# Kernel optimization log

Measured on AMD Instinct MI355X. Metric: run time of the kernel, lower is better.

The kernel has to match this reference:

```python
import jax, jax.numpy as jnp
import numpy as np

N = 8192
NFEAT = 784
NUM_CLASSES = 10


def _glorot(key, shape):
    lim = 1.0 / np.sqrt(shape[0])
    return jax.random.uniform(key, shape, jnp.float32, -lim, lim)


def setup_inputs() -> dict:
    key = jax.random.key(0)
    ks = jax.random.split(key, 16)
    x = jax.random.normal(ks[0], (N, NFEAT), jnp.float32)
    adj = (jax.random.uniform(ks[1], (N, N)) < 0.02).astype(jnp.float32)
    adj = jnp.maximum(adj, jnp.eye(N, dtype=jnp.float32))
    dims = [(NFEAT, 256), (256, 128), (256, 256), (128, 128), (128, 128),
            (128, 64), (128, 128), (128, 128), (128, 1)]
    names = ['gcn1', 'd11', 'd12', 'gcn2', 'd21', 'd22', 'gcn3', 'd31', 'd32']
    inp = {'x': x, 'adj': adj}
    for i, (nm, (fi, fo)) in enumerate(zip(names, dims)):
        inp['W_' + nm] = _glorot(ks[2 + i], (fi, fo))
        inp['b_' + nm] = jnp.zeros((fo,), jnp.float32)
    inp['W_fc'] = _glorot(ks[11], (128, NUM_CLASSES))
    inp['b_fc'] = jnp.zeros((NUM_CLASSES,), jnp.float32)
    return inp


def _gcn(x, adj, W, b):
    # Kipf GCN layer: adj @ (x @ W) + b
    return adj @ (x @ W) + b


def _normalize_adj(adj):
    # degree[i,i] = 1/nnz(row_i); out = sqrt(D) @ adj @ sqrt(D)
    deg = jnp.sum(adj != 0, axis=1).astype(adj.dtype)  # [N]
    d = jax.lax.rsqrt(deg)                              # 1/sqrt(deg)
    return adj * d[:, None] * d[None, :]


def reference(x, adj,
              W_gcn1, b_gcn1, W_d11, b_d11, W_d12, b_d12,
              W_gcn2, b_gcn2, W_d21, b_d21, W_d22, b_d22,
              W_gcn3, b_gcn3, W_d31, b_d31, W_d32, b_d32,
              W_fc, b_fc):
    adj = _normalize_adj(adj)
    x = _gcn(x, adj, W_gcn1, b_gcn1)                  # [N, 256]
    z1 = _gcn(x, adj, W_d11, b_d11)                   # [N, 128]
    s1 = jax.nn.softmax(_gcn(x, adj, W_d12, b_d12), axis=1)  # [N, 256]
    x = s1.T @ z1                                     # [256, 128]
    adj = s1.T @ adj @ s1                             # [256, 256]
    x = _gcn(x, adj, W_gcn2, b_gcn2)                  # [256, 128]
    z2 = _gcn(x, adj, W_d21, b_d21)                   # [256, 128]
    s2 = jax.nn.softmax(_gcn(x, adj, W_d22, b_d22), axis=1)  # [256, 64]
    x = s2.T @ z2                                     # [64, 128]
    adj = s2.T @ (adj @ s2)                           # [64, 64]
    x = _gcn(x, adj, W_gcn3, b_gcn3)                  # [64, 128]
    z3 = _gcn(x, adj, W_d31, b_d31)                   # [64, 128]
    s3 = jax.nn.softmax(_gcn(x, adj, W_d32, b_d32), axis=1)  # [64, 1]
    x = s3.T @ z3                                     # [1, 128]
    out = x @ W_fc + b_fc                             # [1, 10]
    return jax.nn.log_softmax(out, axis=1)
```

## Files before the change

kernel.cpp:

```cpp
#include <hip/hip_runtime.h>
#include <hip/hip_bf16.h>
#include <math.h>

#define NROWS 8192
#define MAXNNZ 512

typedef __attribute__((ext_vector_type(8))) short short8v;
typedef __attribute__((ext_vector_type(4))) float floatx4;

__device__ inline void storev(float* p, float v) { *p = v; }
__device__ inline void storev(__hip_bfloat16* p, float v) { *p = __float2bfloat16(v); }

__global__ void build_csr_kernel(const float* __restrict__ adj, int* __restrict__ cols,
                                 int* __restrict__ cnt, float* __restrict__ dvec) {
    int row = blockIdx.x;
    __shared__ int lcnt;
    if (threadIdx.x == 0) lcnt = 0;
    __syncthreads();
    const float* arow = adj + (size_t)row * NROWS;
    int* crow = cols + (size_t)row * MAXNNZ;
    int tid = threadIdx.x;
#pragma unroll
    for (int j = 0; j < NROWS / 1024; ++j) {
        int c = (j * 256 + tid) * 4;
        float4 v = *reinterpret_cast<const float4*>(&arow[c]);
        if (v.x != 0.0f) { int p = atomicAdd(&lcnt, 1); if (p < MAXNNZ) crow[p] = c; }
        if (v.y != 0.0f) { int p = atomicAdd(&lcnt, 1); if (p < MAXNNZ) crow[p] = c + 1; }
        if (v.z != 0.0f) { int p = atomicAdd(&lcnt, 1); if (p < MAXNNZ) crow[p] = c + 2; }
        if (v.w != 0.0f) { int p = atomicAdd(&lcnt, 1); if (p < MAXNNZ) crow[p] = c + 3; }
    }
    __syncthreads();
    if (threadIdx.x == 0) {
        int n = lcnt; if (n > MAXNNZ) n = MAXNNZ;
        cnt[row] = n;
        dvec[row] = rsqrtf((float)lcnt);
    }
}

__global__ void cast_x_kernel(const float* __restrict__ x, __hip_bfloat16* __restrict__ xb) {
    int row = blockIdx.x;
    int tid = threadIdx.x;
    const float* src = x + (size_t)row * 784;
    __hip_bfloat16* dst = xb + (size_t)row * 800;
    for (int c = tid; c < 800; c += 256)
        dst[c] = (c < 784) ? __float2bfloat16(src[c]) : __float2bfloat16(0.0f);
}

__global__ void prep_kernel(const float* __restrict__ Wg1,
                            const float* __restrict__ Wd11, const float* __restrict__ Wd12,
                            const float* __restrict__ bd11, const float* __restrict__ bd12,
                            const float* __restrict__ Wd21, const float* __restrict__ Wd22,
                            const float* __restrict__ bd21, const float* __restrict__ bd22,
                            __hip_bfloat16* __restrict__ Wg1T, __hip_bfloat16* __restrict__ Wcat1T,
                            float* __restrict__ bcat1, float* __restrict__ Wcat2,
                            float* __restrict__ bcat2) {
    int idx = blockIdx.x * 256 + threadIdx.x;
    if (idx < 256 * 800) {
        int n = idx / 800, k = idx % 800;
        Wg1T[idx] = __float2bfloat16(k < 784 ? Wg1[k * 256 + n] : 0.0f);
        return;
    }
    idx -= 256 * 800;
    if (idx < 384 * 256) {
        int n = idx / 256, k = idx % 256;
        float v = (n < 128) ? Wd11[k * 128 + n] : Wd12[k * 256 + (n - 128)];
        Wcat1T[idx] = __float2bfloat16(v);
        return;
    }
    idx -= 384 * 256;
    if (idx < 384) { bcat1[idx] = (idx < 128) ? bd11[idx] : bd12[idx - 128]; return; }
    idx -= 384;
    if (idx < 128 * 192) {
        int r = idx / 192, c = idx % 192;
        Wcat2[idx] = (c < 128) ? Wd21[r * 128 + c] : Wd22[r * 64 + (c - 128)];
        return;
    }
    idx -= 128 * 192;
    if (idx < 192) { bcat2[idx] = (idx < 128) ? bd21[idx] : bd22[idx - 128]; return; }
}

template<typename OUT>
__global__ void gemm_mfma_kernel(const __hip_bfloat16* __restrict__ A,
                                 const __hip_bfloat16* __restrict__ BT,
                                 const float* __restrict__ bias,
                                 OUT* __restrict__ C, int K,
                                 int lda, int ldb, int ldc) {
    __shared__ __hip_bfloat16 As[128][40];
    __shared__ __hip_bfloat16 Bs[64][40];
    int tid = threadIdx.x;
    int w = tid >> 6, lane = tid & 63;
    int row0 = blockIdx.y * 128, col0 = blockIdx.x * 64;
    int lrow = lane & 15, kb = (lane >> 4) * 8;
    floatx4 acc[2][4] = {};
    int ar = tid >> 1, akh = (tid & 1) * 16;
    int bn = tid >> 2, bkh = (tid & 3) * 8;
    for (int k0 = 0; k0 < K; k0 += 32) {
        {
            const float4* src = reinterpret_cast<const float4*>(&A[(size_t)(row0 + ar) * lda + k0 + akh]);
            float4 v0 = src[0], v1 = src[1];
            *reinterpret_cast<float4*>(&As[ar][akh]) = v0;
            *reinterpret_cast<float4*>(&As[ar][akh + 8]) = v1;
        }
        {
            float4 v = *reinterpret_cast<const float4*>(&BT[(size_t)(col0 + bn) * ldb + k0 + bkh]);
            *reinterpret_cast<float4*>(&Bs[bn][bkh]) = v;
        }
        __syncthreads();
        short8v af[2], bf[4];
#pragma unroll
        for (int mi = 0; mi < 2; ++mi)
            af[mi] = *reinterpret_cast<const short8v*>(&As[w * 32 + mi * 16 + lrow][kb]);
#pragma unroll
        for (int ni = 0; ni < 4; ++ni)
            bf[ni] = *reinterpret_cast<const short8v*>(&Bs[ni * 16 + lrow][kb]);
#pragma unroll
        for (int mi = 0; mi < 2; ++mi)
#pragma unroll
            for (int ni = 0; ni < 4; ++ni)
                acc[mi][ni] = __builtin_amdgcn_mfma_f32_16x16x32_bf16(af[mi], bf[ni], acc[mi][ni], 0, 0, 0);
        __syncthreads();
    }
#pragma unroll
    for (int mi = 0; mi < 2; ++mi) {
#pragma unroll
        for (int ni = 0; ni < 4; ++ni) {
            int gcol = col0 + ni * 16 + (lane & 15);
            float bb = bias ? bias[gcol] : 0.0f;
#pragma unroll
            for (int r = 0; r < 4; ++r) {
                int grow = row0 + w * 32 + mi * 16 + (lane >> 4) * 4 + r;
                storev(&C[(size_t)grow * ldc + gcol], acc[mi][ni][r] + bb);
            }
        }
    }
}

template<typename TOUT>
__global__ void spmm_bf16_kernel(const int* __restrict__ cols, const int* __restrict__ cnt,
                                 const float* __restrict__ dvec,
                                 const __hip_bfloat16* __restrict__ H,
                                 const float* __restrict__ bias, TOUT* __restrict__ out,
                                 int ldh, int ldo) {
    int row = blockIdx.x;
    int tid = threadIdx.x;
    __shared__ int sidx[MAXNNZ];
    __shared__ float sw[MAXNNZ];
    int n = cnt[row];
    const int* crow = cols + (size_t)row * MAXNNZ;
    for (int i = tid; i < n; i += 256) {
        int c = crow[i];
        sidx[i] = c * ldh;
        sw[i] = dvec[c];
    }
    __syncthreads();
    float acc = 0.0f;
    int i = 0;
    for (; i + 4 <= n; i += 4) {
        float h0 = __bfloat162float(H[sidx[i]   + tid]);
        float h1 = __bfloat162float(H[sidx[i+1] + tid]);
        float h2 = __bfloat162float(H[sidx[i+2] + tid]);
        float h3 = __bfloat162float(H[sidx[i+3] + tid]);
        acc += sw[i]*h0 + sw[i+1]*h1 + sw[i+2]*h2 + sw[i+3]*h3;
    }
    for (; i < n; i++) acc += sw[i] * __bfloat162float(H[sidx[i] + tid]);
    float r = dvec[row] * acc;
    if (bias) r += bias[tid];
    storev(&out[(size_t)row * ldo + tid], r);
}

__global__ void gemm_bias_kernel(const float* __restrict__ A, const float* __restrict__ B,
                                 const float* __restrict__ bias, float* __restrict__ C,
                                 int M, int N, int K, int lda, int ldb, int ldc) {
    __shared__ float As[16][68];
    __shared__ float Bs[16][68];
    int tx = threadIdx.x, ty = threadIdx.y;
    int tid = ty * 16 + tx;
    int row0 = blockIdx.y * 64, col0 = blockIdx.x * 64;
    int am = tid >> 2, ak = (tid & 3) * 4;
    int bk = tid >> 4, bn = (tid & 15) * 4;
    float acc[4][4] = {};
    for (int k0 = 0; k0 < K; k0 += 16) {
        int gm = row0 + am;
        float4 va = make_float4(0.f, 0.f, 0.f, 0.f);
        if (gm < M) va = *reinterpret_cast<const float4*>(&A[(size_t)gm * lda + k0 + ak]);
        As[ak + 0][am] = va.x; As[ak + 1][am] = va.y;
        As[ak + 2][am] = va.z; As[ak + 3][am] = va.w;
        float4 vb = *reinterpret_cast<const float4*>(&B[(size_t)(k0 + bk) * ldb + col0 + bn]);
        *reinterpret_cast<float4*>(&Bs[bk][bn]) = vb;
        __syncthreads();
#pragma unroll
        for (int k = 0; k < 16; ++k) {
            float4 a = *reinterpret_cast<const float4*>(&As[k][ty * 4]);
            float4 b = *reinterpret_cast<const float4*>(&Bs[k][tx * 4]);
            float av[4] = {a.x, a.y, a.z, a.w};
            float bv[4] = {b.x, b.y, b.z, b.w};
#pragma unroll
            for (int i = 0; i < 4; ++i)
#pragma unroll
                for (int j = 0; j < 4; ++j)
                    acc[i][j] += av[i] * bv[j];
        }
        __syncthreads();
    }
    float4 bb = make_float4(0.f, 0.f, 0.f, 0.f);
    if (bias) bb = *reinterpret_cast<const float4*>(&bias[col0 + tx * 4]);
#pragma unroll
    for (int i = 0; i < 4; ++i) {
        int gm = row0 + ty * 4 + i;
        if (gm >= M) continue;
        float4 v = make_float4(acc[i][0] + bb.x, acc[i][1] + bb.y,
                               acc[i][2] + bb.z, acc[i][3] + bb.w);
        *reinterpret_cast<float4*>(&C[(size_t)gm * ldc + col0 + tx * 4]) = v;
    }
}

__global__ void gemm_atn_kernel(const float* __restrict__ A, const float* __restrict__ B,
                                float* __restrict__ C, int M, int N, int K, int KC,
                                int lda, int ldb, int ldc) {
    __shared__ float As[16][68];
    __shared__ float Bs[16][68];
    int tx = threadIdx.x, ty = threadIdx.y;
    int tid = ty * 16 + tx;
    int row0 = blockIdx.y * 64, col0 = blockIdx.x * 64;
    int kbeg = blockIdx.z * KC;
    int kend = kbeg + KC; if (kend > K) kend = K;
    int ka = tid >> 4, m4 = (tid & 15) * 4;
    int bk = tid >> 4, bn = (tid & 15) * 4;
    float acc[4][4] = {};
    for (int k0 = kbeg; k0 < kend; k0 += 16) {
        int gm = row0 + m4;
        float4 va = make_float4(0.f, 0.f, 0.f, 0.f);
        if (gm < M) va = *reinterpret_cast<const float4*>(&A[(size_t)(k0 + ka) * lda + gm]);
        *reinterpret_cast<float4*>(&As[ka][m4]) = va;
        float4 vb = *reinterpret_cast<const float4*>(&B[(size_t)(k0 + bk) * ldb + col0 + bn]);
        *reinterpret_cast<float4*>(&Bs[bk][bn]) = vb;
        __syncthreads();
#pragma unroll
        for (int k = 0; k < 16; ++k) {
            float4 a = *reinterpret_cast<const float4*>(&As[k][ty * 4]);
            float4 b = *reinterpret_cast<const float4*>(&Bs[k][tx * 4]);
            float av[4] = {a.x, a.y, a.z, a.w};
            float bv[4] = {b.x, b.y, b.z, b.w};
#pragma unroll
            for (int i = 0; i < 4; ++i)
#pragma unroll
                for (int j = 0; j < 4; ++j)
                    acc[i][j] += av[i] * bv[j];
        }
        __syncthreads();
    }
#pragma unroll
    for (int i = 0; i < 4; ++i) {
        int gm = row0 + ty * 4 + i;
        if (gm >= M) continue;
#pragma unroll
        for (int j = 0; j < 4; ++j)
            atomicAdd(&C[(size_t)gm * ldc + col0 + tx * 4 + j], acc[i][j]);
    }
}

__global__ void softmax_rows_kernel(float* __restrict__ data, int NC, int ld, int off,
                                    __hip_bfloat16* __restrict__ bout, int ldb) {
    int row = blockIdx.x;
    float* p = data + (size_t)row * ld + off;
    __shared__ float red[256];
    int tid = threadIdx.x;
    float m = -INFINITY;
    for (int c = tid; c < NC; c += 256) m = fmaxf(m, p[c]);
    red[tid] = m; __syncthreads();
    for (int s = 128; s > 0; s >>= 1) {
        if (tid < s) red[tid] = fmaxf(red[tid], red[tid + s]);
        __syncthreads();
    }
    m = red[0]; __syncthreads();
    float sum = 0.0f;
    for (int c = tid; c < NC; c += 256) sum += expf(p[c] - m);
    red[tid] = sum; __syncthreads();
    for (int s = 128; s > 0; s >>= 1) {
        if (tid < s) red[tid] += red[tid + s];
        __syncthreads();
    }
    float inv = 1.0f / red[0];
    for (int c = tid; c < NC; c += 256) {
        float v = expf(p[c] - m) * inv;
        p[c] = v;
        if (bout) bout[(size_t)row * ldb + c] = __float2bfloat16(v);
    }
}

__global__ void final_kernel(const float* __restrict__ z3, const float* __restrict__ Wfc,
                             const float* __restrict__ bfc, float* __restrict__ out) {
    __shared__ float v[128];
    __shared__ float o[10];
    int tid = threadIdx.x;
    float a = 0.0f;
#pragma unroll
    for (int i = 0; i < 64; i++) a += z3[i * 128 + tid];
    v[tid] = a;
    __syncthreads();
    if (tid < 10) {
        float s = 0.0f;
        for (int k = 0; k < 128; k++) s += v[k] * Wfc[k * 10 + tid];
        o[tid] = s + bfc[tid];
    }
    __syncthreads();
    if (tid == 0) {
        float m = -INFINITY;
        for (int c = 0; c < 10; c++) m = fmaxf(m, o[c]);
        float s = 0.0f;
        for (int c = 0; c < 10; c++) s += expf(o[c] - m);
        float lse = m + logf(s);
        for (int c = 0; c < 10; c++) out[c] = o[c] - lse;
    }
}

extern "C" void kernel_launch(void* const* d_in, const int* in_sizes, int n_in,
                              void* d_out, int out_size, void* d_ws, size_t ws_size,
                              hipStream_t stream) {
    const float* x      = (const float*)d_in[0];
    const float* adj    = (const float*)d_in[1];
    const float* W_gcn1 = (const float*)d_in[2];
    const float* b_gcn1 = (const float*)d_in[3];
    const float* W_d11  = (const float*)d_in[4];
    const float* b_d11  = (const float*)d_in[5];
    const float* W_d12  = (const float*)d_in[6];
    const float* b_d12  = (const float*)d_in[7];
    const float* W_gcn2 = (const float*)d_in[8];
    const float* b_gcn2 = (const float*)d_in[9];
    const float* W_d21  = (const float*)d_in[10];
    const float* b_d21  = (const float*)d_in[11];
    const float* W_d22  = (const float*)d_in[12];
    const float* b_d22  = (const float*)d_in[13];
    const float* W_gcn3 = (const float*)d_in[14];
    const float* b_gcn3 = (const float*)d_in[15];
    const float* W_d31  = (const float*)d_in[16];
    const float* b_d31  = (const float*)d_in[17];
    const float* W_fc   = (const float*)d_in[20];
    const float* b_fc   = (const float*)d_in[21];

    char* ws = (char*)d_ws;
    size_t off = 0;
    auto alloc = [&](size_t bytes) -> char* {
        char* p = ws + off;
        off = (off + bytes + 255) & ~(size_t)255;
        return p;
    };
    int*   cols  = (int*)  alloc((size_t)NROWS * MAXNNZ * 4);
    int*   cnt   = (int*)  alloc((size_t)NROWS * 4);
    float* dvec  = (float*)alloc((size_t)NROWS * 4);
    __hip_bfloat16* xb     = (__hip_bfloat16*)alloc((size_t)NROWS * 800 * 2);
    __hip_bfloat16* Wg1T   = (__hip_bfloat16*)alloc(256 * 800 * 2);
    __hip_bfloat16* Wcat1T = (__hip_bfloat16*)alloc(384 * 256 * 2);
    __hip_bfloat16* XW1b   = (__hip_bfloat16*)alloc((size_t)NROWS * 256 * 2);
    __hip_bfloat16* x1b    = (__hip_bfloat16*)alloc((size_t)NROWS * 256 * 2);
    __hip_bfloat16* u1b    = (__hip_bfloat16*)alloc((size_t)NROWS * 256 * 2);
    __hip_bfloat16* ASb    = (__hip_bfloat16*)alloc((size_t)NROWS * 256 * 2);
    float* Tcat  = (float*)alloc((size_t)NROWS * 384 * 4);
    float* s1    = (float*)alloc((size_t)NROWS * 256 * 4);
    float* Xp    = (float*)alloc(256 * 128 * 4);
    float* adj2  = (float*)alloc(256 * 256 * 4);
    float* Xp2   = (float*)alloc(64 * 128 * 4);
    float* adj3  = (float*)alloc(64 * 64 * 4);
    size_t zero_bytes = 256*128*4 + 256*256*4 + 64*128*4 + 64*64*4;
    float* XW2   = (float*)alloc(256 * 128 * 4);
    float* x2    = (float*)alloc(256 * 128 * 4);
    float* T2cat = (float*)alloc(256 * 192 * 4);
    float* Z2cat = (float*)alloc(256 * 192 * 4);
    float* AS2   = (float*)alloc(256 * 64 * 4);
    float* T30   = (float*)alloc(64 * 128 * 4);
    float* x3    = (float*)alloc(64 * 128 * 4);
    float* T31   = (float*)alloc(64 * 128 * 4);
    float* z3    = (float*)alloc(64 * 128 * 4);
    float* Wcat2 = (float*)alloc(128 * 192 * 4);
    float* bcat1 = (float*)alloc(384 * 4);
    float* bcat2 = (float*)alloc(192 * 4);

    dim3 blk2(16, 16);

    prep_kernel<<<(256*800 + 384*256 + 384 + 128*192 + 192 + 255) / 256, 256, 0, stream>>>(
        W_gcn1, W_d11, W_d12, b_d11, b_d12, W_d21, W_d22, b_d21, b_d22,
        Wg1T, Wcat1T, bcat1, Wcat2, bcat2);
    cast_x_kernel<<<NROWS, 256, 0, stream>>>(x, xb);
    hipMemsetAsync(Xp, 0, zero_bytes, stream);
    build_csr_kernel<<<NROWS, 256, 0, stream>>>(adj, cols, cnt, dvec);

    gemm_mfma_kernel<__hip_bfloat16><<<dim3(4, 64), 256, 0, stream>>>(
        xb, Wg1T, nullptr, XW1b, 800, 800, 800, 256);
    spmm_bf16_kernel<__hip_bfloat16><<<NROWS, 256, 0, stream>>>(
        cols, cnt, dvec, XW1b, b_gcn1, x1b, 256, 256);
    spmm_bf16_kernel<__hip_bfloat16><<<NROWS, 256, 0, stream>>>(
        cols, cnt, dvec, x1b, nullptr, u1b, 256, 256);
    gemm_mfma_kernel<float><<<dim3(6, 64), 256, 0, stream>>>(
        u1b, Wcat1T, bcat1, Tcat, 256, 256, 256, 384);
    softmax_rows_kernel<<<NROWS, 256, 0, stream>>>(Tcat, 256, 384, 128, ASb, 256);
    spmm_bf16_kernel<float><<<NROWS, 256, 0, stream>>>(
        cols, cnt, dvec, ASb, nullptr, s1, 256, 256);

    gemm_atn_kernel<<<dim3(2, 4, 32), blk2, 0, stream>>>(Tcat + 128, Tcat, Xp,
                                                         256, 128, NROWS, 256, 384, 384, 128);
    gemm_atn_kernel<<<dim3(4, 4, 32), blk2, 0, stream>>>(Tcat + 128, s1, adj2,
                                                         256, 256, NROWS, 256, 384, 256, 256);

    gemm_bias_kernel<<<dim3(2, 4), blk2, 0, stream>>>(Xp, W_gcn2, nullptr, XW2,
                                                      256, 128, 128, 128, 128, 128);
    gemm_bias_kernel<<<dim3(2, 4), blk2, 0, stream>>>(adj2, XW2, b_gcn2, x2,
                                                      256, 128, 256, 256, 128, 128);
    gemm_bias_kernel<<<dim3(3, 4), blk2, 0, stream>>>(x2, Wcat2, nullptr, T2cat,
                                                      256, 192, 128, 128, 192, 192);
    gemm_bias_kernel<<<dim3(3, 4), blk2, 0, stream>>>(adj2, T2cat, bcat2, Z2cat,
                                                      256, 192, 256, 256, 192, 192);
    softmax_rows_kernel<<<256, 256, 0, stream>>>(Z2cat, 64, 192, 128, nullptr, 0);
    gemm_bias_kernel<<<dim3(1, 4), blk2, 0, stream>>>(adj2, Z2cat + 128, nullptr, AS2,
                                                      256, 64, 256, 256, 192, 64);
    gemm_atn_kernel<<<dim3(2, 1, 1), blk2, 0, stream>>>(Z2cat + 128, Z2cat, Xp2,
                                                        64, 128, 256, 256, 192, 192, 128);
    gemm_atn_kernel<<<dim3(1, 1, 1), blk2, 0, stream>>>(Z2cat + 128, AS2, adj3,
                                                        64, 64, 256, 256, 192, 64, 64);

    gemm_bias_kernel<<<dim3(2, 1), blk2, 0, stream>>>(Xp2, W_gcn3, nullptr, T30,
                                                      64, 128, 128, 128, 128, 128);
    gemm_bias_kernel<<<dim3(2, 1), blk2, 0, stream>>>(adj3, T30, b_gcn3, x3,
                                                      64, 128, 64, 64, 128, 128);
    gemm_bias_kernel<<<dim3(2, 1), blk2, 0, stream>>>(x3, W_d31, nullptr, T31,
                                                      64, 128, 128, 128, 128, 128);
    gemm_bias_kernel<<<dim3(2, 1), blk2, 0, stream>>>(adj3, T31, b_d31, z3,
                                                      64, 128, 64, 64, 128, 128);
    final_kernel<<<1, 128, 0, stream>>>(z3, W_fc, b_fc, (float*)d_out);
}
```

Measured before the change: 871.5 us.

## Move first-level pooling path to bf16 with MFMA transposed GEMMs and sliced SpMM

The Tcat/s1 intermediates change from fp32 to bf16, and a new softmax kernel reads and writes bf16. The pooling products s1^T z1 and s1^T (A s1) now run on a new MFMA-based transposed-A GEMM with split-K and atomics, replacing the fp32 scalar kernel. SpMM is split across two column slices of 128 threads per row, with the gather loop unrolled by 8. The aim is to cut memory traffic and use matrix cores for the large N=8192 reductions, at the cost of lower precision in the softmax and assignment values.

```diff
diff --git a/kernel.cpp b/kernel.cpp
--- a/kernel.cpp
+++ b/kernel.cpp
@@ -135,37 +135,114 @@
     }
 }
 
-template<typename TOUT>
-__global__ void spmm_bf16_kernel(const int* __restrict__ cols, const int* __restrict__ cnt,
-                                 const float* __restrict__ dvec,
-                                 const __hip_bfloat16* __restrict__ H,
-                                 const float* __restrict__ bias, TOUT* __restrict__ out,
-                                 int ldh, int ldo) {
+__global__ void gemm_atn_mfma_kernel(const __hip_bfloat16* __restrict__ A,
+                                     const __hip_bfloat16* __restrict__ B,
+                                     float* __restrict__ C, int M, int N, int K, int KC,
+                                     int lda, int ldb, int ldc) {
+    __shared__ unsigned short At[64][40];
+    __shared__ unsigned short Bt[64][40];
+    int tid = threadIdx.x;
+    int w = tid >> 6, lane = tid & 63;
+    int m0 = blockIdx.y * 64, n0 = blockIdx.x * 64;
+    int kbeg = blockIdx.z * KC;
+    int kend = kbeg + KC; if (kend > K) kend = K;
+    int lrow = lane & 15, kb = (lane >> 4) * 8;
+    floatx4 acc[4] = {};
+    int kk = tid >> 3;
+    int eg = (tid & 7) * 8;
+    for (int k0 = kbeg; k0 < kend; k0 += 32) {
+        {
+            unsigned short v[8];
+            *reinterpret_cast<float4*>(v) = *reinterpret_cast<const float4*>(
+                &A[(size_t)(k0 + kk) * lda + m0 + eg]);
+#pragma unroll
+            for (int e = 0; e < 8; ++e) At[eg + e][kk] = v[e];
+        }
+        {
+            unsigned short v[8];
+            *reinterpret_cast<float4*>(v) = *reinterpret_cast<const float4*>(
+                &B[(size_t)(k0 + kk) * ldb + n0 + eg]);
+#pragma unroll
+            for (int e = 0; e < 8; ++e) Bt[eg + e][kk] = v[e];
+        }
+        __syncthreads();
+        short8v af = *reinterpret_cast<const short8v*>(&At[w * 16 + lrow][kb]);
+#pragma unroll
+        for (int ni = 0; ni < 4; ++ni) {
+            short8v bfr = *reinterpret_cast<const short8v*>(&Bt[ni * 16 + lrow][kb]);
+            acc[ni] = __builtin_amdgcn_mfma_f32_16x16x32_bf16(af, bfr, acc[ni], 0, 0, 0);
+        }
+        __syncthreads();
+    }
+#pragma unroll
+    for (int ni = 0; ni < 4; ++ni) {
+        int gcol = n0 + ni * 16 + lrow;
+#pragma unroll
+        for (int r = 0; r < 4; ++r) {
+            int grow = m0 + w * 16 + (lane >> 4) * 4 + r;
+            atomicAdd(&C[(size_t)grow * ldc + gcol], acc[ni][r]);
+        }
+    }
+}
+
+__global__ void spmm_bf16_sliced_kernel(const int* __restrict__ cols, const int* __restrict__ cnt,
+                                        const float* __restrict__ dvec,
+                                        const __hip_bfloat16* __restrict__ H,
+                                        const float* __restrict__ bias,
+                                        __hip_bfloat16* __restrict__ out,
+                                        int ldh, int ldo) {
     int row = blockIdx.x;
+    int cb = blockIdx.y * 128;
     int tid = threadIdx.x;
     __shared__ int sidx[MAXNNZ];
     __shared__ float sw[MAXNNZ];
     int n = cnt[row];
     const int* crow = cols + (size_t)row * MAXNNZ;
-    for (int i = tid; i < n; i += 256) {
+    for (int i = tid; i < n; i += 128) {
         int c = crow[i];
-        sidx[i] = c * ldh;
+        sidx[i] = c * ldh + cb;
         sw[i] = dvec[c];
     }
     __syncthreads();
     float acc = 0.0f;
     int i = 0;
-    for (; i + 4 <= n; i += 4) {
+    for (; i + 8 <= n; i += 8) {
         float h0 = __bfloat162float(H[sidx[i]   + tid]);
         float h1 = __bfloat162float(H[sidx[i+1] + tid]);
         float h2 = __bfloat162float(H[sidx[i+2] + tid]);
         float h3 = __bfloat162float(H[sidx[i+3] + tid]);
-        acc += sw[i]*h0 + sw[i+1]*h1 + sw[i+2]*h2 + sw[i+3]*h3;
+        float h4 = __bfloat162float(H[sidx[i+4] + tid]);
+        float h5 = __bfloat162float(H[sidx[i+5] + tid]);
+        float h6 = __bfloat162float(H[sidx[i+6] + tid]);
+        float h7 = __bfloat162float(H[sidx[i+7] + tid]);
+        acc += sw[i]*h0 + sw[i+1]*h1 + sw[i+2]*h2 + sw[i+3]*h3
+             + sw[i+4]*h4 + sw[i+5]*h5 + sw[i+6]*h6 + sw[i+7]*h7;
     }
     for (; i < n; i++) acc += sw[i] * __bfloat162float(H[sidx[i] + tid]);
     float r = dvec[row] * acc;
-    if (bias) r += bias[tid];
-    storev(&out[(size_t)row * ldo + tid], r);
+    if (bias) r += bias[cb + tid];
+    out[(size_t)row * ldo + cb + tid] = __float2bfloat16(r);
+}
+
+__global__ void softmax_bf16_kernel(const __hip_bfloat16* __restrict__ in,
+                                    __hip_bfloat16* __restrict__ out) {
+    int row = blockIdx.x;
+    int tid = threadIdx.x;
+    __shared__ float red[256];
+    float v = __bfloat162float(in[(size_t)row * 384 + 128 + tid]);
+    red[tid] = v; __syncthreads();
+    for (int s = 128; s > 0; s >>= 1) {
+        if (tid < s) red[tid] = fmaxf(red[tid], red[tid + s]);
+        __syncthreads();
+    }
+    float m = red[0]; __syncthreads();
+    float e = expf(v - m);
+    red[tid] = e; __syncthreads();
+    for (int s = 128; s > 0; s >>= 1) {
+        if (tid < s) red[tid] += red[tid + s];
+        __syncthreads();
+    }
+    out[(size_t)row * 256 + tid] = __float2bfloat16(e / red[0]);
 }
 
 __global__ void gemm_bias_kernel(const float* __restrict__ A, const float* __restrict__ B,
@@ -259,8 +336,7 @@
     }
 }
 
-__global__ void softmax_rows_kernel(float* __restrict__ data, int NC, int ld, int off,
-                                    __hip_bfloat16* __restrict__ bout, int ldb) {
+__global__ void softmax_rows_kernel(float* __restrict__ data, int NC, int ld, int off) {
     int row = blockIdx.x;
     float* p = data + (size_t)row * ld + off;
     __shared__ float red[256];
@@ -281,11 +357,7 @@
         __syncthreads();
     }
     float inv = 1.0f / red[0];
-    for (int c = tid; c < NC; c += 256) {
-        float v = expf(p[c] - m) * inv;
-        p[c] = v;
-        if (bout) bout[(size_t)row * ldb + c] = __float2bfloat16(v);
-    }
+    for (int c = tid; c < NC; c += 256) p[c] = expf(p[c] - m) * inv;
 }
 
 __global__ void final_kernel(const float* __restrict__ z3, const float* __restrict__ Wfc,
@@ -354,9 +426,9 @@
     __hip_bfloat16* XW1b   = (__hip_bfloat16*)alloc((size_t)NROWS * 256 * 2);
     __hip_bfloat16* x1b    = (__hip_bfloat16*)alloc((size_t)NROWS * 256 * 2);
     __hip_bfloat16* u1b    = (__hip_bfloat16*)alloc((size_t)NROWS * 256 * 2);
+    __hip_bfloat16* zcatb  = (__hip_bfloat16*)alloc((size_t)NROWS * 384 * 2);
     __hip_bfloat16* ASb    = (__hip_bfloat16*)alloc((size_t)NROWS * 256 * 2);
-    float* Tcat  = (float*)alloc((size_t)NROWS * 384 * 4);
-    float* s1    = (float*)alloc((size_t)NROWS * 256 * 4);
+    __hip_bfloat16* s1b    = (__hip_bfloat16*)alloc((size_t)NROWS * 256 * 2);
     float* Xp    = (float*)alloc(256 * 128 * 4);
     float* adj2  = (float*)alloc(256 * 256 * 4);
     float* Xp2   = (float*)alloc(64 * 128 * 4);
@@ -386,20 +458,20 @@
 
     gemm_mfma_kernel<__hip_bfloat16><<<dim3(4, 64), 256, 0, stream>>>(
         xb, Wg1T, nullptr, XW1b, 800, 800, 800, 256);
-    spmm_bf16_kernel<__hip_bfloat16><<<NROWS, 256, 0, stream>>>(
+    spmm_bf16_sliced_kernel<<<dim3(NROWS, 2), 128, 0, stream>>>(
         cols, cnt, dvec, XW1b, b_gcn1, x1b, 256, 256);
-    spmm_bf16_kernel<__hip_bfloat16><<<NROWS, 256, 0, stream>>>(
+    spmm_bf16_sliced_kernel<<<dim3(NROWS, 2), 128, 0, stream>>>(
         cols, cnt, dvec, x1b, nullptr, u1b, 256, 256);
-    gemm_mfma_kernel<float><<<dim3(6, 64), 256, 0, stream>>>(
-        u1b, Wcat1T, bcat1, Tcat, 256, 256, 256, 384);
-    softmax_rows_kernel<<<NROWS, 256, 0, stream>>>(Tcat, 256, 384, 128, ASb, 256);
-    spmm_bf16_kernel<float><<<NROWS, 256, 0, stream>>>(
-        cols, cnt, dvec, ASb, nullptr, s1, 256, 256);
-
-    gemm_atn_kernel<<<dim3(2, 4, 32), blk2, 0, stream>>>(Tcat + 128, Tcat, Xp,
-                                                         256, 128, NROWS, 256, 384, 384, 128);
-    gemm_atn_kernel<<<dim3(4, 4, 32), blk2, 0, stream>>>(Tcat + 128, s1, adj2,
-                                                         256, 256, NROWS, 256, 384, 256, 256);
+    gemm_mfma_kernel<__hip_bfloat16><<<dim3(6, 64), 256, 0, stream>>>(
+        u1b, Wcat1T, bcat1, zcatb, 256, 256, 256, 384);
+    softmax_bf16_kernel<<<NROWS, 256, 0, stream>>>(zcatb, ASb);
+    spmm_bf16_sliced_kernel<<<dim3(NROWS, 2), 128, 0, stream>>>(
+        cols, cnt, dvec, ASb, nullptr, s1b, 256, 256);
+
+    gemm_atn_mfma_kernel<<<dim3(2, 4, 16), 256, 0, stream>>>(
+        ASb, zcatb, Xp, 256, 128, NROWS, 512, 256, 384, 128);
+    gemm_atn_mfma_kernel<<<dim3(4, 4, 16), 256, 0, stream>>>(
+        ASb, s1b, adj2, 256, 256, NROWS, 512, 256, 256, 256);
 
     gemm_bias_kernel<<<dim3(2, 4), blk2, 0, stream>>>(Xp, W_gcn2, nullptr, XW2,
                                                       256, 128, 128, 128, 128, 128);
@@ -409,7 +481,7 @@
                                                       256, 192, 128, 128, 192, 192);
     gemm_bias_kernel<<<dim3(3, 4), blk2, 0, stream>>>(adj2, T2cat, bcat2, Z2cat,
                                                       256, 192, 256, 256, 192, 192);
-    softmax_rows_kernel<<<256, 256, 0, stream>>>(Z2cat, 64, 192, 128, nullptr, 0);
+    softmax_rows_kernel<<<256, 256, 0, stream>>>(Z2cat, 64, 192, 128);
     gemm_bias_kernel<<<dim3(1, 4), blk2, 0, stream>>>(adj2, Z2cat + 128, nullptr, AS2,
                                                       256, 64, 256, 256, 192, 64);
     gemm_atn_kernel<<<dim3(2, 1, 1), blk2, 0, stream>>>(Z2cat + 128, Z2cat, Xp2,
```

Measured after the change: 819.7 us. 1.06x faster.
